# Kernel optimization log

Measured on AMD Instinct MI355X. Metric: run time of the kernel, lower is better.

Reference implementation:

```python
import jax, jax.numpy as jnp
import numpy as np

LAMBDA_COORD = 5.0
LAMBDA_NOOBJ = 0.5
B, N, F = 2048, 64, 19  # batch, nb_pred, 2 + n_classes


def _greedy_scan(Permut, v, h, D2, mask, n):
    # One greedy-assignment phase: n sequential argmax/one-hot steps.
    def step(carry, _):
        Permut, v, h, D2 = carry
        D2 = D2 * v[:, :, None] * h[:, None, :]
        A = jax.nn.one_hot(jnp.argmax(D2, axis=-1), n, dtype=D2.dtype)          # row-wise best col
        Bm = v[:, :, None] * A * D2
        C = jnp.swapaxes(jax.nn.one_hot(jnp.argmax(Bm, axis=-2), n, dtype=D2.dtype), -1, -2)  # col-wise best row
        E = v[:, :, None] * A * C
        Permut = Permut + E
        v = (1.0 - Permut.sum(-1)) * mask
        h = 1.0 - Permut.sum(-2)
        return (Permut, v, h, D2), None
    (Permut, v, h, D2), _ = jax.lax.scan(step, (Permut, v, h, D2), None, length=n)
    return Permut, v, h, D2


def _permute_ypred(y_true, y_pred):
    alpha = y_true[:, :, 0]                      # [B, N] in {0,1}
    x = y_true[:, :, 1]
    p = y_pred[:, :, 1]
    n = x.shape[-1]
    D1 = 1.0 - jnp.abs(x[:, :, None] - p[:, None, :])   # [B, N, N] similarity

    # Phase 1: match ground-truth positives (rows with alpha=1).
    Permut0 = jnp.zeros_like(D1)
    v0 = alpha
    h0 = jnp.ones_like(alpha)
    D2_0 = v0[:, :, None] * D1
    Permut, v, h, _ = _greedy_scan(Permut0, v0, h0, D2_0, alpha, n)

    # Phase 2: match remaining rows (alpha=0) to remaining predictions.
    neg = 1.0 - alpha
    D2_1 = neg[:, :, None] * D1 * h[:, None, :]
    Permut, _, _, _ = _greedy_scan(Permut, neg, h, D2_1, neg, n)

    permutation = jnp.argmax(Permut, axis=-1)            # [B, N]
    idx = jnp.broadcast_to(permutation[:, :, None], y_pred.shape)
    return jnp.take_along_axis(y_pred, idx, axis=1)


def setup_inputs() -> dict:
    key = jax.random.key(0)
    k1, k2, k3 = jax.random.split(key, 3)
    y_true = jax.random.uniform(k1, (B, N, F), dtype=jnp.float32)
    alpha = (jax.random.uniform(k3, (B, N)) < 0.3).astype(jnp.float32)
    y_true = y_true.at[:, :, 0].set(alpha)
    y_pred = jax.random.uniform(k2, (B, N, F), dtype=jnp.float32)
    return {"y_true": y_true, "y_pred": y_pred}


def reference(y_true, y_pred):
    y_pred = _permute_ypred(y_true, y_pred)
    a = y_true[:, :, 0]
    loss = jnp.sum(
        a * LAMBDA_COORD * jnp.square(y_true[:, :, 1] - y_pred[:, :, 1])
        + a * jnp.square(a - y_pred[:, :, 0])
        + (1.0 - a) * LAMBDA_NOOBJ * jnp.square(a - y_pred[:, :, 0])
        + a * jnp.sum(jnp.square(y_true[:, :, 2:] - y_pred[:, :, 2:]), axis=-1)
    )
    return loss
```

## Files before the change

kernel.cpp:

```cpp
#include <hip/hip_runtime.h>
#include <stdint.h>


#define NN 64
#define NF 19
#define ROWF (NN * NF)
#define ROW4 (ROWF / 4)

__global__ __launch_bounds__(64) void spotting_loss_kernel(
    const float* __restrict__ yt, const float* __restrict__ yp,
    float* __restrict__ out)
{
  const int b = blockIdx.x;
  const int i = threadIdx.x;

  __shared__ float yt_sh[ROWF];
  __shared__ float yp_sh[ROWF];
  __shared__ float p_sh[NN];
  __shared__ unsigned long long key_sh[NN];

  const float4* __restrict__ yt4 = (const float4*)(yt + (size_t)b * ROWF);
  const float4* __restrict__ yp4 = (const float4*)(yp + (size_t)b * ROWF);
  float4* yt_sh4 = (float4*)yt_sh;
  float4* yp_sh4 = (float4*)yp_sh;
#pragma unroll
  for (int t = 0; t < 5; ++t) {
    const int idx = t * NN + i;
    if (idx < ROW4) {
      yt_sh4[idx] = yt4[idx];
      yp_sh4[idx] = yp4[idx];
    }
  }
  key_sh[i] = 0ull;
  __syncthreads();

  const float alpha = yt_sh[i * NF + 0];
  const float x     = yt_sh[i * NF + 1];
  p_sh[i] = yp_sh[i * NF + 1];
  __syncthreads();

  float D1r[NN];
  const float4* __restrict__ p4 = (const float4*)p_sh;
#pragma unroll
  for (int j4 = 0; j4 < NN / 4; ++j4) {
    const float4 pv = p4[j4];
    D1r[4 * j4 + 0] = 1.0f - fabsf(x - pv.x);
    D1r[4 * j4 + 1] = 1.0f - fabsf(x - pv.y);
    D1r[4 * j4 + 2] = 1.0f - fabsf(x - pv.z);
    D1r[4 * j4 + 3] = 1.0f - fabsf(x - pv.w);
  }

  unsigned long long hbits = ~0ull;
  int perm = 0, jmax = 0;
  float best = 0.0f;
  unsigned tag = 0;

  for (int phase = 0; phase < 2; ++phase) {
    bool vlive  = (phase == 0) ? (alpha > 0.5f) : (alpha < 0.5f);
    bool rescan = vlive;

    for (int it = 0; it < NN; ++it) {
      if (__ballot(vlive) == 0ull) break;
      ++tag;

      if (rescan) {
        const unsigned hlo = (unsigned)hbits;
        const unsigned hhi = (unsigned)(hbits >> 32);
        best = -1.0f; jmax = 0;
#pragma unroll
        for (int j = 0; j < NN; ++j) {
          const unsigned bit = (j < 32) ? ((hlo >> j) & 1u)
                                        : ((hhi >> (j - 32)) & 1u);
          const float t = __uint_as_float(__float_as_uint(D1r[j]) & (0u - bit));
          if (t > best) { best = t; jmax = j; }
        }
        rescan = false;
      }

      if (vlive && best > 0.0f) {
        const unsigned long long key =
            ((unsigned long long)tag << 38) |
            ((unsigned long long)__float_as_uint(best) << 6) |
            (unsigned long long)(63 - i);
        atomicMax(&key_sh[jmax], key);
      }
      __builtin_amdgcn_wave_barrier();

      const unsigned long long kc = key_sh[i];
      const unsigned long long killed =
          __ballot((unsigned)(kc >> 38) == tag);

      if (vlive && best > 0.0f) {
        const unsigned long long kw = key_sh[jmax];
        if ((int)(63ull - (kw & 63ull)) == i) {
          perm = jmax;
          vlive = false;
        } else if ((killed >> jmax) & 1ull) {
          rescan = true;
        }
      }
      hbits &= ~killed;
      __builtin_amdgcn_wave_barrier();
    }
  }

  const float a = alpha;
  const int pbase = perm * NF;
  const float p0 = yp_sh[pbase + 0];
  const float p1 = yp_sh[pbase + 1];
  const float dx = x - p1;
  const float da = a - p0;
  float s2 = 0.0f;
#pragma unroll
  for (int f = 2; f < NF; ++f) {
    const float d = yt_sh[i * NF + f] - yp_sh[pbase + f];
    s2 += d * d;
  }
  float l = a * 5.0f * (dx * dx)
          + a * (da * da)
          + (1.0f - a) * 0.5f * (da * da)
          + a * s2;

#pragma unroll
  for (int off = 32; off > 0; off >>= 1) l += __shfl_down(l, off);
  if (i == 0) atomicAdd(out, l);
}

extern "C" void kernel_launch(void* const* d_in, const int* in_sizes, int n_in,
                              void* d_out, int out_size, void* d_ws, size_t ws_size,
                              hipStream_t stream) {
  const float* yt = (const float*)d_in[0];
  const float* yp = (const float*)d_in[1];
  float* out = (float*)d_out;
  const int B = in_sizes[0] / ROWF;

  hipMemsetAsync(out, 0, sizeof(float) * (size_t)out_size, stream);
  spotting_loss_kernel<<<B, 64, 0, stream>>>(yt, yp, out);
}
```

Measured before the change: 108.9 us.

## Use tree-reduced argmax, drop y_true staging, simplify auction bookkeeping

Measured after the change: 110.5 us. Within noise of the previous version (+1.5%).

```diff
diff --git a/kernel.cpp b/kernel.cpp
--- a/kernel.cpp
+++ b/kernel.cpp
@@ -7,51 +7,41 @@
 #define ROWF (NN * NF)
 #define ROW4 (ROWF / 4)
 
-__global__ __launch_bounds__(64) void spotting_loss_kernel(
+__device__ __forceinline__ unsigned umin2(unsigned a, unsigned b) {
+  return a < b ? a : b;
+}
+
+__global__ __launch_bounds__(64, 2) void spotting_loss_kernel(
     const float* __restrict__ yt, const float* __restrict__ yp,
     float* __restrict__ out)
 {
   const int b = blockIdx.x;
   const int i = threadIdx.x;
 
-  __shared__ float yt_sh[ROWF];
   __shared__ float yp_sh[ROWF];
-  __shared__ float p_sh[NN];
   __shared__ unsigned long long key_sh[NN];
 
-  const float4* __restrict__ yt4 = (const float4*)(yt + (size_t)b * ROWF);
+  const float* __restrict__ ytb = yt + (size_t)b * ROWF;
   const float4* __restrict__ yp4 = (const float4*)(yp + (size_t)b * ROWF);
-  float4* yt_sh4 = (float4*)yt_sh;
   float4* yp_sh4 = (float4*)yp_sh;
 #pragma unroll
   for (int t = 0; t < 5; ++t) {
     const int idx = t * NN + i;
-    if (idx < ROW4) {
-      yt_sh4[idx] = yt4[idx];
-      yp_sh4[idx] = yp4[idx];
-    }
+    if (idx < ROW4) yp_sh4[idx] = yp4[idx];
   }
   key_sh[i] = 0ull;
+  const float alpha = ytb[i * NF + 0];
+  const float x     = ytb[i * NF + 1];
   __syncthreads();
 
-  const float alpha = yt_sh[i * NF + 0];
-  const float x     = yt_sh[i * NF + 1];
-  p_sh[i] = yp_sh[i * NF + 1];
-  __syncthreads();
-
-  float D1r[NN];
-  const float4* __restrict__ p4 = (const float4*)p_sh;
+  float D1v[NN];
 #pragma unroll
-  for (int j4 = 0; j4 < NN / 4; ++j4) {
-    const float4 pv = p4[j4];
-    D1r[4 * j4 + 0] = 1.0f - fabsf(x - pv.x);
-    D1r[4 * j4 + 1] = 1.0f - fabsf(x - pv.y);
-    D1r[4 * j4 + 2] = 1.0f - fabsf(x - pv.z);
-    D1r[4 * j4 + 3] = 1.0f - fabsf(x - pv.w);
-  }
+  for (int j = 0; j < NN; ++j)
+    D1v[j] = 1.0f - fabsf(x - yp_sh[j * NF + 1]);
 
   unsigned long long hbits = ~0ull;
   int perm = 0, jmax = 0;
+  unsigned long long mykey = 0;
   float best = 0.0f;
   unsigned tag = 0;
 
@@ -64,38 +54,57 @@
       ++tag;
 
       if (rescan) {
-        const unsigned hlo = (unsigned)hbits;
-        const unsigned hhi = (unsigned)(hbits >> 32);
-        best = -1.0f; jmax = 0;
+        float m[NN];
 #pragma unroll
-        for (int j = 0; j < NN; ++j) {
-          const unsigned bit = (j < 32) ? ((hlo >> j) & 1u)
-                                        : ((hhi >> (j - 32)) & 1u);
-          const float t = __uint_as_float(__float_as_uint(D1r[j]) & (0u - bit));
-          if (t > best) { best = t; jmax = j; }
+        for (int j = 0; j < NN; ++j)
+          m[j] = ((hbits >> j) & 1ull) ? D1v[j] : 0.0f;
+
+        float t32[32], t16[16], t8[8], t4[4];
+#pragma unroll
+        for (int j = 0; j < 32; ++j) t32[j] = fmaxf(m[j], m[j + 32]);
+#pragma unroll
+        for (int j = 0; j < 16; ++j) t16[j] = fmaxf(t32[j], t32[j + 16]);
+#pragma unroll
+        for (int j = 0; j < 8; ++j)  t8[j]  = fmaxf(t16[j], t16[j + 8]);
+#pragma unroll
+        for (int j = 0; j < 4; ++j)  t4[j]  = fmaxf(t8[j], t8[j + 4]);
+        best = fmaxf(fmaxf(t4[0], t4[1]), fmaxf(t4[2], t4[3]));
+
+        unsigned c32[32], c16[16], c8[8], c4[4];
+#pragma unroll
+        for (int j = 0; j < 32; ++j) {
+          const unsigned a0 = (m[j]      == best) ? (unsigned)j        : 255u;
+          const unsigned a1 = (m[j + 32] == best) ? (unsigned)(j + 32) : 255u;
+          c32[j] = umin2(a0, a1);
         }
+#pragma unroll
+        for (int j = 0; j < 16; ++j) c16[j] = umin2(c32[j], c32[j + 16]);
+#pragma unroll
+        for (int j = 0; j < 8; ++j)  c8[j]  = umin2(c16[j], c16[j + 8]);
+#pragma unroll
+        for (int j = 0; j < 4; ++j)  c4[j]  = umin2(c8[j], c8[j + 4]);
+        jmax = (int)umin2(umin2(c4[0], c4[1]), umin2(c4[2], c4[3]));
         rescan = false;
       }
 
-      if (vlive && best > 0.0f) {
-        const unsigned long long key =
-            ((unsigned long long)tag << 38) |
-            ((unsigned long long)__float_as_uint(best) << 6) |
-            (unsigned long long)(63 - i);
-        atomicMax(&key_sh[jmax], key);
+      if (vlive) {
+        mykey = ((unsigned long long)tag << 38) |
+                ((unsigned long long)__float_as_uint(best) << 6) |
+                (unsigned long long)(63 - i);
+        atomicMax(&key_sh[jmax], mykey);
       }
       __builtin_amdgcn_wave_barrier();
 
       const unsigned long long kc = key_sh[i];
+      const unsigned long long kw = key_sh[jmax];
       const unsigned long long killed =
           __ballot((unsigned)(kc >> 38) == tag);
 
-      if (vlive && best > 0.0f) {
-        const unsigned long long kw = key_sh[jmax];
-        if ((int)(63ull - (kw & 63ull)) == i) {
+      if (vlive) {
+        if (kw == mykey) {
           perm = jmax;
           vlive = false;
-        } else if ((killed >> jmax) & 1ull) {
+        } else {
           rescan = true;
         }
       }
@@ -113,7 +122,7 @@
   float s2 = 0.0f;
 #pragma unroll
   for (int f = 2; f < NF; ++f) {
-    const float d = yt_sh[i * NF + f] - yp_sh[pbase + f];
+    const float d = ytb[i * NF + f] - yp_sh[pbase + f];
     s2 += d * d;
   }
   float l = a * 5.0f * (dx * dx)
```
